# Kernel tuning notes

Hardware: AMD Instinct MI355X
Metric: run time of the kernel (lower is better)

## Reference

```python
import jax, jax.numpy as jnp
import numpy as np

FEAT = 256      # config.feature_size
HID = 256       # config.hidden_size
MAXC = 10       # config.max_child_num
NSEM = 64       # Tree.num_sem
B = 32768       # number of parent nodes (one batched tree level)


def _forward(box_input, eps, W_box, b_box, W1, b1, W2, b2,
             Ws1, bs1, Wmu, bmu, Wvar, bvar, sem_ids, n_children):
    # ---- BoxEncoder on every leaf child: relu(Linear(10 -> FEAT)) ----
    leaf = jax.nn.relu(jnp.einsum('bmi,if->bmf', box_input, W_box) + b_box)  # [B,M,FEAT]
    # ---- concat semantic one-hot per child ----
    sem = jax.nn.one_hot(sem_ids, NSEM, dtype=leaf.dtype)                    # [B,M,NSEM]
    child_feats = jnp.concatenate([leaf, sem], axis=-1)                      # [B,M,FEAT+NSEM]
    # ---- SymmetricChildEncoder ----
    feat = jax.nn.relu(jnp.einsum('bmf,fh->bmh', child_feats, W1) + b1)      # [B,M,HID]
    exists = (jnp.arange(MAXC) < n_children[:, None]).astype(feat.dtype)[..., None]  # [B,M,1]
    x = jnp.max(feat * exists, axis=1)                                       # [B,HID]
    parent_feat = jax.nn.relu(x @ W2 + b2)                                   # [B,FEAT]
    # ---- Sampler (variational, probabilistic) ----
    enc = jax.nn.relu(parent_feat @ Ws1 + bs1)                               # [B,HID]
    mu = enc @ Wmu + bmu                                                     # [B,FEAT]
    logvar = enc @ Wvar + bvar                                               # [B,FEAT]
    std = jnp.exp(0.5 * logvar)
    kld = 1.0 + logvar - mu * mu - jnp.exp(logvar)
    return jnp.concatenate([eps * std + mu, kld], axis=1)                    # [B,2*FEAT]


def setup_inputs() -> dict:
    key = jax.random.key(0)
    ks = jax.random.split(key, 16)
    def lin_w(k, fan_in, shape):
        return (jax.random.normal(k, shape, jnp.float32) / np.sqrt(fan_in)).astype(jnp.float32)
    return {
        'box_input': jax.random.normal(ks[0], (B, MAXC, 10), jnp.float32),
        'eps': jax.random.normal(ks[1], (B, FEAT), jnp.float32),
        'W_box': lin_w(ks[2], 10, (10, FEAT)),
        'b_box': jnp.zeros((FEAT,), jnp.float32),
        'W1': lin_w(ks[3], FEAT + NSEM, (FEAT + NSEM, HID)),
        'b1': jnp.zeros((HID,), jnp.float32),
        'W2': lin_w(ks[4], HID, (HID, FEAT)),
        'b2': jnp.zeros((FEAT,), jnp.float32),
        'Ws1': lin_w(ks[5], FEAT, (FEAT, HID)),
        'bs1': jnp.zeros((HID,), jnp.float32),
        'Wmu': lin_w(ks[6], HID, (HID, FEAT)),
        'bmu': jnp.zeros((FEAT,), jnp.float32),
        'Wvar': lin_w(ks[7], HID, (HID, FEAT)),
        'bvar': jnp.zeros((FEAT,), jnp.float32),
        'sem_ids': jax.random.randint(ks[8], (B, MAXC), 0, NSEM, jnp.int32),
        'n_children': jax.random.randint(ks[9], (B,), 1, MAXC + 1, jnp.int32),
    }


def reference(box_input, eps, W_box, b_box, W1, b1, W2, b2,
              Ws1, bs1, Wmu, bmu, Wvar, bvar, sem_ids, n_children):
    return _forward(box_input, eps, W_box, b_box, W1, b1, W2, b2,
                    Ws1, bs1, Wmu, bmu, Wvar, bvar, sem_ids, n_children)
```

## Files before the change

kernel.cpp:

```cpp
#include <hip/hip_runtime.h>
#include <math.h>


#define NPAR  32768
#define LDA1  328
#define LDA2  264
#define W1F_OFF   0
#define W2F_OFF   81920
#define WBX_OFF   (81920 + 4*65536)
#define XBUF_OFF  (WBX_OFF + 8192)

typedef _Float16 f16;
typedef _Float16 f16x8 __attribute__((ext_vector_type(8)));
typedef float    f32x4 __attribute__((ext_vector_type(4)));

__device__ __forceinline__ void async16(const void* g, void* l) {
    __builtin_amdgcn_global_load_lds((const __attribute__((address_space(1))) void*)g,
                                     (__attribute__((address_space(3))) void*)l, 16, 0, 0);
}
__device__ __forceinline__ f32x4 mfma16(f16x8 a, f16x8 b, f32x4 c) {
    return __builtin_amdgcn_mfma_f32_16x16x32_f16(a, b, c, 0, 0, 0);
}

__global__ void kconv(const float* __restrict__ W1, const float* __restrict__ W2,
                      const float* __restrict__ Ws1, const float* __restrict__ Wmu,
                      const float* __restrict__ Wvar, const float* __restrict__ Wbox,
                      f16* __restrict__ ws) {
    int idx = blockIdx.x * 256 + threadIdx.x;
    if (idx < 81920) {
        int j = idx & 7, lane = (idx >> 3) & 63, t = idx >> 9;
        int c = t % 10, n16 = t / 10;
        int k = c * 32 + (lane >> 4) * 8 + j;
        int n = n16 * 16 + (lane & 15);
        ws[idx] = (f16)W1[k * 256 + n];
    } else if (idx < WBX_OFF) {
        int r = idx - 81920;
        int wsel = r >> 16, r2 = r & 65535;
        const float* s = (wsel == 0) ? W2 : (wsel == 1) ? Ws1 : (wsel == 2) ? Wmu : Wvar;
        int j = r2 & 7, lane = (r2 >> 3) & 63, c = (r2 >> 9) & 7, n16 = r2 >> 12;
        int k = c * 32 + (lane >> 4) * 8 + j;
        int n = n16 * 16 + (lane & 15);
        ws[idx] = (f16)s[k * 256 + n];
    } else if (idx < XBUF_OFF) {
        int r = idx - WBX_OFF;
        int j = r & 7, lane = (r >> 3) & 63, n16 = r >> 9;
        int k = (lane >> 4) * 8 + j;
        int n = n16 * 16 + (lane & 15);
        ws[idx] = (f16)((k < 10) ? Wbox[k * 256 + n] : 0.f);
    }
}

__global__ __launch_bounds__(256, 2)
void k1(const float* __restrict__ box, const float* __restrict__ bbox,
        const float* __restrict__ b1, const int* __restrict__ sem,
        const int* __restrict__ nch, const f16* __restrict__ wsh,
        f16* __restrict__ xbuf) {
    __shared__ __align__(16) f16 lA[80 * LDA1];
    __shared__ int lnc[8];

    int tid = threadIdx.x, blk = blockIdx.x;
    int w = tid >> 6, lane = tid & 63, q = lane >> 4, r16 = lane & 15;
    const f16* w1f = wsh + W1F_OFF;
    const f16* wbxf = wsh + WBX_OFF;

    if (tid < 8) lnc[tid] = nch[blk * 8 + tid];

    float bbv[4], b1v[4];
    #pragma unroll
    for (int nt = 0; nt < 4; nt++) {
        int col = w * 64 + nt * 16 + r16;
        bbv[nt] = bbox[col];
        b1v[nt] = b1[col];
    }

    f32x4 acc[5][4];
    {
        f16x8 bb[4], ab[5];
        #pragma unroll
        for (int nt = 0; nt < 4; nt++)
            bb[nt] = *(const f16x8*)&wbxf[((w * 4 + nt) * 64 + lane) * 8];
        #pragma unroll
        for (int mt = 0; mt < 5; mt++) {
            const float* bp = box + (size_t)blk * 800 + (mt * 16 + r16) * 10;
            float v[8] = {0.f, 0.f, 0.f, 0.f, 0.f, 0.f, 0.f, 0.f};
            if (q == 0) {
                float2 t0 = *(const float2*)(bp + 0), t1 = *(const float2*)(bp + 2);
                float2 t2 = *(const float2*)(bp + 4), t3 = *(const float2*)(bp + 6);
                v[0] = t0.x; v[1] = t0.y; v[2] = t1.x; v[3] = t1.y;
                v[4] = t2.x; v[5] = t2.y; v[6] = t3.x; v[7] = t3.y;
            } else if (q == 1) {
                float2 t = *(const float2*)(bp + 8);
                v[0] = t.x; v[1] = t.y;
            }
            f16x8 t;
            #pragma unroll
            for (int j = 0; j < 8; j++) t[j] = (f16)v[j];
            ab[mt] = t;
        }
        #pragma unroll
        for (int mt = 0; mt < 5; mt++)
            #pragma unroll
            for (int nt = 0; nt < 4; nt++)
                acc[mt][nt] = mfma16(ab[mt], bb[nt], (f32x4){0.f, 0.f, 0.f, 0.f});
    }
    #pragma unroll
    for (int mt = 0; mt < 5; mt++) {
        #pragma unroll
        for (int i = 0; i < 4; i++) {
            int r = mt * 16 + q * 4 + i;
            int p = (r * 205) >> 11;
            int d = (r - 10 * p) * 8 + p;
            #pragma unroll
            for (int nt = 0; nt < 4; nt++) {
                int col = w * 64 + nt * 16 + r16;
                lA[d * LDA1 + col] = (f16)fmaxf(acc[mt][nt][i] + bbv[nt], 0.f);
            }
        }
    }
    if (tid < 80) {
        int p8 = tid & 7, m8 = tid >> 3;
        int sid = sem[blk * 80 + p8 * 10 + m8];
        f16x8 z = {(f16)0.f, (f16)0.f, (f16)0.f, (f16)0.f, (f16)0.f, (f16)0.f, (f16)0.f, (f16)0.f};
        #pragma unroll
        for (int j = 0; j < 8; j++) *(f16x8*)&lA[tid * LDA1 + 256 + j * 8] = z;
        lA[tid * LDA1 + 256 + sid] = (f16)1.f;
    }

    #pragma unroll
    for (int mt = 0; mt < 5; mt++)
        #pragma unroll
        for (int nt = 0; nt < 4; nt++) acc[mt][nt] = (f32x4){0.f, 0.f, 0.f, 0.f};

    f16x8 bs[3][4];
    auto loadB = [&](int c, int s) {
        #pragma unroll
        for (int nt = 0; nt < 4; nt++)
            bs[s][nt] = *(const f16x8*)&w1f[(((w * 4 + nt) * 10 + c) * 64 + lane) * 8];
    };
    loadB(0, 0); loadB(1, 1); loadB(2, 2);
    __syncthreads();
    #pragma unroll
    for (int c = 0; c < 10; c++) {
        f16x8 a[5];
        #pragma unroll
        for (int mt = 0; mt < 5; mt++)
            a[mt] = *(const f16x8*)&lA[(mt * 16 + r16) * LDA1 + c * 32 + q * 8];
        int s = c % 3;
        #pragma unroll
        for (int mt = 0; mt < 5; mt++)
            #pragma unroll
            for (int nt = 0; nt < 4; nt++) acc[mt][nt] = mfma16(a[mt], bs[s][nt], acc[mt][nt]);
        if (c + 3 < 10) loadB(c + 3, s);
    }

    int qh = q >> 1, qb = q & 1;
    int ncv[4];
    #pragma unroll
    for (int i = 0; i < 4; i++) ncv[i] = lnc[4 * qb + i];
    float pm[4][4];
    #pragma unroll
    for (int i = 0; i < 4; i++)
        #pragma unroll
        for (int nt = 0; nt < 4; nt++) pm[i][nt] = 0.f;
    #pragma unroll
    for (int mt = 0; mt < 5; mt++) {
        int m = 2 * mt + qh;
        #pragma unroll
        for (int i = 0; i < 4; i++) {
            bool live = m < ncv[i];
            #pragma unroll
            for (int nt = 0; nt < 4; nt++) {
                float v = fmaxf(acc[mt][nt][i] + b1v[nt], 0.f);
                pm[i][nt] = fmaxf(pm[i][nt], live ? v : 0.f);
            }
        }
    }
    #pragma unroll
    for (int i = 0; i < 4; i++)
        #pragma unroll
        for (int nt = 0; nt < 4; nt++)
            pm[i][nt] = fmaxf(pm[i][nt], __shfl_xor(pm[i][nt], 32, 64));
    if (q < 2) {
        #pragma unroll
        for (int i = 0; i < 4; i++) {
            size_t row = (size_t)blk * 8 + 4 * q + i;
            #pragma unroll
            for (int nt = 0; nt < 4; nt++)
                xbuf[row * LDA2 + w * 64 + nt * 16 + r16] = (f16)pm[i][nt];
        }
    }
}

__global__ __launch_bounds__(256, 2)
void k2(const f16* __restrict__ xbuf, const f16* __restrict__ wsh,
        const float* __restrict__ b2, const float* __restrict__ bs1,
        const float* __restrict__ bmu, const float* __restrict__ bvar,
        const float* __restrict__ eps, float* __restrict__ out) {
    __shared__ __align__(16) f16 actA[32 * LDA2];
    __shared__ __align__(16) f16 actB[32 * LDA2];

    int tid = threadIdx.x, blk = blockIdx.x;
    int w = tid >> 6, lane = tid & 63, q = lane >> 4, r16 = lane & 15;
    const f16* w2f   = wsh + W2F_OFF;
    const f16* ws1f  = w2f + 65536;
    const f16* wmuf  = w2f + 2 * 65536;
    const f16* wvarf = w2f + 3 * 65536;

    float b2v[4], bs1v[4], bmv[4], bvv[4];
    #pragma unroll
    for (int nt = 0; nt < 4; nt++) {
        int col = w * 64 + nt * 16 + r16;
        b2v[nt] = b2[col]; bs1v[nt] = bs1[col];
        bmv[nt] = bmu[col]; bvv[nt] = bvar[col];
    }

    {
        const char* src = (const char*)(xbuf + (size_t)blk * 32 * LDA2);
        #pragma unroll
        for (int j = 0; j < 5; j++) {
            int idx = tid + j * 256;
            if (idx < 1056) async16(src + idx * 16, (char*)actA + idx * 16);
        }
    }

    f32x4 acc[2][4];
    f16x8 bs[3][4];
    auto loadB = [&](const f16* wt, int c, int s) {
        #pragma unroll
        for (int nt = 0; nt < 4; nt++)
            bs[s][nt] = *(const f16x8*)&wt[(((w * 4 + nt) * 8 + c) * 64 + lane) * 8];
    };
    auto gemm = [&](const f16* A, const f16* wt) {
        #pragma unroll
        for (int mt = 0; mt < 2; mt++)
            #pragma unroll
            for (int nt = 0; nt < 4; nt++) acc[mt][nt] = (f32x4){0.f, 0.f, 0.f, 0.f};
        #pragma unroll
        for (int c = 0; c < 8; c++) {
            f16x8 a[2];
            #pragma unroll
            for (int mt = 0; mt < 2; mt++)
                a[mt] = *(const f16x8*)&A[(mt * 16 + r16) * LDA2 + c * 32 + q * 8];
            int s = c % 3;
            #pragma unroll
            for (int mt = 0; mt < 2; mt++)
                #pragma unroll
                for (int nt = 0; nt < 4; nt++) acc[mt][nt] = mfma16(a[mt], bs[s][nt], acc[mt][nt]);
            if (c + 3 < 8) loadB(wt, c + 3, s);
        }
    };

    loadB(w2f, 0, 0); loadB(w2f, 1, 1); loadB(w2f, 2, 2);
    __syncthreads();
    gemm(actA, w2f);
    #pragma unroll
    for (int nt = 0; nt < 4; nt++) {
        int col = w * 64 + nt * 16 + r16;
        #pragma unroll
        for (int mt = 0; mt < 2; mt++)
            #pragma unroll
            for (int i = 0; i < 4; i++)
                actB[(mt * 16 + q * 4 + i) * LDA2 + col] = (f16)fmaxf(acc[mt][nt][i] + b2v[nt], 0.f);
    }
    loadB(ws1f, 0, 0); loadB(ws1f, 1, 1); loadB(ws1f, 2, 2);
    __syncthreads();

    gemm(actB, ws1f);
    #pragma unroll
    for (int nt = 0; nt < 4; nt++) {
        int col = w * 64 + nt * 16 + r16;
        #pragma unroll
        for (int mt = 0; mt < 2; mt++)
            #pragma unroll
            for (int i = 0; i < 4; i++)
                actA[(mt * 16 + q * 4 + i) * LDA2 + col] = (f16)fmaxf(acc[mt][nt][i] + bs1v[nt], 0.f);
    }
    loadB(wmuf, 0, 0); loadB(wmuf, 1, 1); loadB(wmuf, 2, 2);
    __syncthreads();

    gemm(actA, wmuf);
    f32x4 mu[2][4];
    #pragma unroll
    for (int mt = 0; mt < 2; mt++)
        #pragma unroll
        for (int nt = 0; nt < 4; nt++) mu[mt][nt] = acc[mt][nt];

    float ev[2][4][4];
    #pragma unroll
    for (int mt = 0; mt < 2; mt++)
        #pragma unroll
        for (int i = 0; i < 4; i++) {
            size_t grow = (size_t)blk * 32 + mt * 16 + q * 4 + i;
            #pragma unroll
            for (int nt = 0; nt < 4; nt++)
                ev[mt][nt][i] = eps[grow * 256 + w * 64 + nt * 16 + r16];
        }

    loadB(wvarf, 0, 0); loadB(wvarf, 1, 1); loadB(wvarf, 2, 2);
    gemm(actA, wvarf);
    #pragma unroll
    for (int mt = 0; mt < 2; mt++)
        #pragma unroll
        for (int nt = 0; nt < 4; nt++) {
            int col = w * 64 + nt * 16 + r16;
            #pragma unroll
            for (int i = 0; i < 4; i++) {
                size_t grow = (size_t)blk * 32 + mt * 16 + q * 4 + i;
                float m_ = mu[mt][nt][i] + bmv[nt];
                float lv = acc[mt][nt][i] + bvv[nt];
                float e  = expf(lv);
                out[grow * 512 + col]       = ev[mt][nt][i] * sqrtf(e) + m_;
                out[grow * 512 + 256 + col] = 1.f + lv - m_ * m_ - e;
            }
        }
}

extern "C" void kernel_launch(void* const* d_in, const int* in_sizes, int n_in,
                              void* d_out, int out_size, void* d_ws, size_t ws_size,
                              hipStream_t stream) {
    const float* box  = (const float*)d_in[0];
    const float* eps  = (const float*)d_in[1];
    const float* Wbox = (const float*)d_in[2];
    const float* bbox = (const float*)d_in[3];
    const float* W1   = (const float*)d_in[4];
    const float* b1   = (const float*)d_in[5];
    const float* W2   = (const float*)d_in[6];
    const float* b2   = (const float*)d_in[7];
    const float* Ws1  = (const float*)d_in[8];
    const float* bs1  = (const float*)d_in[9];
    const float* Wmu  = (const float*)d_in[10];
    const float* bmu  = (const float*)d_in[11];
    const float* Wvar = (const float*)d_in[12];
    const float* bvar = (const float*)d_in[13];
    const int*   sem  = (const int*)d_in[14];
    const int*   nch  = (const int*)d_in[15];

    f16* wsh  = (f16*)d_ws;
    f16* xbuf = wsh + XBUF_OFF;

    kconv<<<XBUF_OFF / 256, 256, 0, stream>>>(W1, W2, Ws1, Wmu, Wvar, Wbox, wsh);
    k1<<<NPAR / 8, 256, 0, stream>>>(box, bbox, b1, sem, nch, wsh, xbuf);
    k2<<<NPAR / 32, 256, 0, stream>>>(xbuf, wsh, b2, bs1, bmu, bvar, eps, (float*)d_out);
}
```

Baseline: 218.8 us.

## Pre-pack box inputs to f16, use K16 MFMA, swizzle LDS, raise occupancy

The box inputs are converted to padded f16 rows inside the conversion kernel, so k1 reads them with one 8-byte load per tile instead of branchy float2 loads and in-kernel conversion. The box encoder now uses a 16x16x16 MFMA with a K=16 packed W_box. The leaf activations are stored into LDS with an XOR-style slot swizzle to reduce bank conflicts on the A-fragment reads. Launch bounds are raised for k1 and k2 to allow more resident blocks. The cost is an extra global round trip for the box data and possible register spills from the tighter bounds.

```diff
diff --git a/kernel.cpp b/kernel.cpp
--- a/kernel.cpp
+++ b/kernel.cpp
@@ -9,9 +9,11 @@
 #define W2F_OFF   81920
 #define WBX_OFF   (81920 + 4*65536)
 #define XBUF_OFF  (WBX_OFF + 8192)
+#define BOXF_OFF  (XBUF_OFF + NPAR*264)
 
 typedef _Float16 f16;
 typedef _Float16 f16x8 __attribute__((ext_vector_type(8)));
+typedef _Float16 f16x4 __attribute__((ext_vector_type(4)));
 typedef float    f32x4 __attribute__((ext_vector_type(4)));
 
 __device__ __forceinline__ void async16(const void* g, void* l) {
@@ -21,11 +23,14 @@
 __device__ __forceinline__ f32x4 mfma16(f16x8 a, f16x8 b, f32x4 c) {
     return __builtin_amdgcn_mfma_f32_16x16x32_f16(a, b, c, 0, 0, 0);
 }
+__device__ __forceinline__ f32x4 mfma16k(f16x4 a, f16x4 b, f32x4 c) {
+    return __builtin_amdgcn_mfma_f32_16x16x16f16(a, b, c, 0, 0, 0);
+}
 
 __global__ void kconv(const float* __restrict__ W1, const float* __restrict__ W2,
                       const float* __restrict__ Ws1, const float* __restrict__ Wmu,
                       const float* __restrict__ Wvar, const float* __restrict__ Wbox,
-                      f16* __restrict__ ws) {
+                      const float* __restrict__ box, f16* __restrict__ ws) {
     int idx = blockIdx.x * 256 + threadIdx.x;
     if (idx < 81920) {
         int j = idx & 7, lane = (idx >> 3) & 63, t = idx >> 9;
@@ -41,17 +46,35 @@
         int k = c * 32 + (lane >> 4) * 8 + j;
         int n = n16 * 16 + (lane & 15);
         ws[idx] = (f16)s[k * 256 + n];
-    } else if (idx < XBUF_OFF) {
+    } else if (idx < WBX_OFF + 4096) {
         int r = idx - WBX_OFF;
-        int j = r & 7, lane = (r >> 3) & 63, n16 = r >> 9;
-        int k = (lane >> 4) * 8 + j;
+        int j = r & 3, lane = (r >> 2) & 63, n16 = r >> 8;
+        int k = (lane >> 4) * 4 + j;
         int n = n16 * 16 + (lane & 15);
         ws[idx] = (f16)((k < 10) ? Wbox[k * 256 + n] : 0.f);
-    }
-}
-
-__global__ __launch_bounds__(256, 2)
-void k1(const float* __restrict__ box, const float* __restrict__ bbox,
+    } else if (idx >= XBUF_OFF) {
+        int row = idx - XBUF_OFF;
+        if (row < NPAR * 10) {
+            const float* bp = box + (size_t)row * 10;
+            float2 v0 = *(const float2*)(bp + 0), v1 = *(const float2*)(bp + 2);
+            float2 v2 = *(const float2*)(bp + 4), v3 = *(const float2*)(bp + 6);
+            float2 v4 = *(const float2*)(bp + 8);
+            f16x8 lo, hi;
+            lo[0] = (f16)v0.x; lo[1] = (f16)v0.y; lo[2] = (f16)v1.x; lo[3] = (f16)v1.y;
+            lo[4] = (f16)v2.x; lo[5] = (f16)v2.y; lo[6] = (f16)v3.x; lo[7] = (f16)v3.y;
+            hi[0] = (f16)v4.x; hi[1] = (f16)v4.y;
+            hi[2] = (f16)0.f; hi[3] = (f16)0.f; hi[4] = (f16)0.f;
+            hi[5] = (f16)0.f; hi[6] = (f16)0.f; hi[7] = (f16)0.f;
+            f16* dst = ws + BOXF_OFF + (size_t)row * 16;
+            *(f16x8*)dst = lo;
+            *(f16x8*)(dst + 8) = hi;
+        }
+    }
+}
+#define KCONV_THREADS (XBUF_OFF + NPAR*10)
+
+__global__ __launch_bounds__(256, 3)
+void k1(const f16* __restrict__ boxf, const float* __restrict__ bbox,
         const float* __restrict__ b1, const int* __restrict__ sem,
         const int* __restrict__ nch, const f16* __restrict__ wsh,
         f16* __restrict__ xbuf) {
@@ -60,6 +83,7 @@
 
     int tid = threadIdx.x, blk = blockIdx.x;
     int w = tid >> 6, lane = tid & 63, q = lane >> 4, r16 = lane & 15;
+    int r3 = r16 >> 3, r7 = r16 & 7;
     const f16* w1f = wsh + W1F_OFF;
     const f16* wbxf = wsh + WBX_OFF;
 
@@ -75,33 +99,18 @@
 
     f32x4 acc[5][4];
     {
-        f16x8 bb[4], ab[5];
+        f16x4 bb4[4], ab4[5];
         #pragma unroll
         for (int nt = 0; nt < 4; nt++)
-            bb[nt] = *(const f16x8*)&wbxf[((w * 4 + nt) * 64 + lane) * 8];
-        #pragma unroll
-        for (int mt = 0; mt < 5; mt++) {
-            const float* bp = box + (size_t)blk * 800 + (mt * 16 + r16) * 10;
-            float v[8] = {0.f, 0.f, 0.f, 0.f, 0.f, 0.f, 0.f, 0.f};
-            if (q == 0) {
-                float2 t0 = *(const float2*)(bp + 0), t1 = *(const float2*)(bp + 2);
-                float2 t2 = *(const float2*)(bp + 4), t3 = *(const float2*)(bp + 6);
-                v[0] = t0.x; v[1] = t0.y; v[2] = t1.x; v[3] = t1.y;
-                v[4] = t2.x; v[5] = t2.y; v[6] = t3.x; v[7] = t3.y;
-            } else if (q == 1) {
-                float2 t = *(const float2*)(bp + 8);
-                v[0] = t.x; v[1] = t.y;
-            }
-            f16x8 t;
-            #pragma unroll
-            for (int j = 0; j < 8; j++) t[j] = (f16)v[j];
-            ab[mt] = t;
-        }
+            bb4[nt] = *(const f16x4*)&wbxf[((w * 4 + nt) * 64 + lane) * 4];
         #pragma unroll
         for (int mt = 0; mt < 5; mt++)
+            ab4[mt] = *(const f16x4*)&boxf[((size_t)blk * 80 + mt * 16 + r16) * 16 + q * 4];
+        #pragma unroll
+        for (int mt = 0; mt < 5; mt++)
             #pragma unroll
             for (int nt = 0; nt < 4; nt++)
-                acc[mt][nt] = mfma16(ab[mt], bb[nt], (f32x4){0.f, 0.f, 0.f, 0.f});
+                acc[mt][nt] = mfma16k(ab4[mt], bb4[nt], (f32x4){0.f, 0.f, 0.f, 0.f});
     }
     #pragma unroll
     for (int mt = 0; mt < 5; mt++) {
@@ -109,11 +118,13 @@
         for (int i = 0; i < 4; i++) {
             int r = mt * 16 + q * 4 + i;
             int p = (r * 205) >> 11;
-            int d = (r - 10 * p) * 8 + p;
+            int m = r - 10 * p;
+            int dbase = (m * 8 + p) * LDA1;
             #pragma unroll
             for (int nt = 0; nt < 4; nt++) {
-                int col = w * 64 + nt * 16 + r16;
-                lA[d * LDA1 + col] = (f16)fmaxf(acc[mt][nt][i] + bbv[nt], 0.f);
+                int ks = w * 8 + nt * 2 + r3;
+                int sp = (ks + 2 * m) & 31;
+                lA[dbase + sp * 8 + r7] = (f16)fmaxf(acc[mt][nt][i] + bbv[nt], 0.f);
             }
         }
     }
@@ -143,8 +154,11 @@
     for (int c = 0; c < 10; c++) {
         f16x8 a[5];
         #pragma unroll
-        for (int mt = 0; mt < 5; mt++)
-            a[mt] = *(const f16x8*)&lA[(mt * 16 + r16) * LDA1 + c * 32 + q * 8];
+        for (int mt = 0; mt < 5; mt++) {
+            int ks = 4 * c + q;
+            int sp = (c < 8) ? ((ks + 4 * mt + 2 * r3) & 31) : ks;
+            a[mt] = *(const f16x8*)&lA[(mt * 16 + r16) * LDA1 + sp * 8];
+        }
         int s = c % 3;
         #pragma unroll
         for (int mt = 0; mt < 5; mt++)
@@ -191,7 +205,7 @@
     }
 }
 
-__global__ __launch_bounds__(256, 2)
+__global__ __launch_bounds__(256, 4)
 void k2(const f16* __restrict__ xbuf, const f16* __restrict__ wsh,
         const float* __restrict__ b2, const float* __restrict__ bs1,
         const float* __restrict__ bmu, const float* __restrict__ bvar,
@@ -337,8 +351,9 @@
 
     f16* wsh  = (f16*)d_ws;
     f16* xbuf = wsh + XBUF_OFF;
-
-    kconv<<<XBUF_OFF / 256, 256, 0, stream>>>(W1, W2, Ws1, Wmu, Wvar, Wbox, wsh);
-    k1<<<NPAR / 8, 256, 0, stream>>>(box, bbox, b1, sem, nch, wsh, xbuf);
+    f16* boxf = wsh + BOXF_OFF;
+
+    kconv<<<KCONV_THREADS / 256, 256, 0, stream>>>(W1, W2, Ws1, Wmu, Wvar, Wbox, box, wsh);
+    k1<<<NPAR / 8, 256, 0, stream>>>(boxf, bbox, b1, sem, nch, wsh, xbuf);
     k2<<<NPAR / 32, 256, 0, stream>>>(xbuf, wsh, b2, bs1, bmu, bvar, eps, (float*)d_out);
 }
```

Result: slower. 243.8 us (+11.4%).
